# Optimization experiments

Hardware: AMD Instinct MI355X
Metric: run time of the kernel (lower is better)

Reference implementation:

```python
import jax, jax.numpy as jnp
import numpy as np

B, S, D, H = 32, 8192, 128, 256  # batch-of-MLPs, seq_len, emb_dim, hidden_dim
LN_EPS = 1e-5


def setup_inputs() -> dict:
    key = jax.random.key(0)
    k0, k1, k2, k3 = jax.random.split(key, 4)
    x = jax.random.normal(k0, (B, S, D), dtype=jnp.float32)
    # shared learned Q projection (torch Linear stores W as [out,in]; y = x @ W.T)
    Wq = jax.random.normal(k1, (D, D), dtype=jnp.float32) / np.float32(np.sqrt(D))
    # per-batch-index (non-shared) fast-weight MLP params
    W1 = jax.random.normal(k2, (B, D, H), dtype=jnp.float32) / np.float32(np.sqrt(D))
    b1 = jnp.zeros((B, H), dtype=jnp.float32)
    W2 = jax.random.normal(k3, (B, H, D), dtype=jnp.float32) / np.float32(np.sqrt(H))
    b2 = jnp.zeros((B, D), dtype=jnp.float32)
    gamma = jnp.ones((B, D), dtype=jnp.float32)
    beta = jnp.zeros((B, D), dtype=jnp.float32)
    return dict(x=x, Wq=Wq, W1=W1, b1=b1, W2=W2, b2=b2, gamma=gamma, beta=beta)


def reference(x, Wq, W1, b1, W2, b2, gamma, beta):
    # queries = silu(Q(x))
    q = jax.nn.silu(jnp.einsum('bsd,ed->bse', x, Wq))
    # torch F.normalize with default dim=1 -> L2-normalize over the sequence axis
    q = q / jnp.clip(jnp.linalg.norm(q, axis=1, keepdims=True), 1e-12)
    # ParallelMLPs: per-index MLP with distinct weights (grouped GEMM), + residual
    h = jax.nn.silu(jnp.einsum('bsd,bdh->bsh', q, W1) + b1[:, None, :])
    o = jnp.einsum('bsh,bhd->bsd', h, W2) + b2[:, None, :]
    mu = jnp.mean(o, axis=-1, keepdims=True)
    var = jnp.mean(jnp.square(o - mu), axis=-1, keepdims=True)
    ln = (o - mu) / jnp.sqrt(var + LN_EPS) * gamma[:, None, :] + beta[:, None, :]
    return ln + q
```

## Files before the change

### kernel.cpp

```cpp
#include <hip/hip_runtime.h>
#include <stdint.h>

#define B_ 32
#define S_ 8192
#define D_ 128
#define H_ 256

typedef __attribute__((ext_vector_type(4))) float f32x4;
typedef __attribute__((ext_vector_type(16))) float f32x16;
typedef __attribute__((ext_vector_type(8))) short bf16x8;
typedef __attribute__((ext_vector_type(4))) unsigned int u32x4;

__device__ __forceinline__ unsigned short f2bf(float f) {
    union { float f; unsigned int u; } v; v.f = f;
    unsigned int r = v.u + 0x7fffu + ((v.u >> 16) & 1u);
    return (unsigned short)(r >> 16);
}
__device__ __forceinline__ float bf2f(unsigned short u) {
    union { unsigned int u; float f; } v; v.u = ((unsigned int)u) << 16;
    return v.f;
}
__device__ __forceinline__ float silu_f(float v) {
    return v * __builtin_amdgcn_rcpf(1.0f + __expf(-v));
}
__device__ __forceinline__ unsigned int cvtpk(float lo, float hi) {
    unsigned int r;
    asm("v_cvt_pk_bf16_f32 %0, %1, %2" : "=v"(r) : "v"(lo), "v"(hi));
    return r;
}
__device__ __forceinline__ void plswap(unsigned int& a, unsigned int& b) {
    asm("v_permlane32_swap_b32 %0, %1" : "+v"(a), "+v"(b));
}
__device__ __forceinline__ void gl16(const void* g, void* l) {
    __builtin_amdgcn_global_load_lds(
        (const __attribute__((address_space(1))) unsigned int*)g,
        (__attribute__((address_space(3))) unsigned int*)l, 16, 0, 0);
}

__global__ void k_prep(const float* __restrict__ Wq, const float* __restrict__ W1,
                       const float* __restrict__ W2, const float* __restrict__ b1,
                       unsigned short* __restrict__ wq_img,
                       unsigned short* __restrict__ wpkg,
                       float* __restrict__ b1r) {
    __shared__ __align__(16) unsigned short tile[8192];
    int t = threadIdx.x, blk = blockIdx.x;
    if (blk < 128) {
        int b = blk >> 2, hc = blk & 3;
#pragma unroll
        for (int i = 0; i < 8; i++) {
            int idx = t + i * 256;
            int d = idx >> 4, hj = idx & 15;
            f32x4 v = *(const f32x4*)(W1 + ((size_t)(b * D_ + d)) * H_ + hc * 64 + hj * 4);
#pragma unroll
            for (int u = 0; u < 4; u++) tile[(hj * 4 + u) * 128 + d] = f2bf(v[u]);
        }
        __syncthreads();
        char* img = (char*)wpkg + (size_t)b * 131072 + (size_t)hc * 32768;
#pragma unroll
        for (int i = 0; i < 4; i++) {
            int c = t + i * 256;
            int n = c >> 9, kk = (c >> 6) & 7, l = c & 63;
            u32x4 v = *(const u32x4*)(tile + (n * 32 + (l & 31)) * 128 + kk * 16 + (l >> 5) * 8);
            *(u32x4*)(img + n * 16384 + kk * 1024 + l * 16) = v;
        }
    } else if (blk < 256) {
        int a = blk - 128;
        int b = a >> 2, hc = a & 3;
#pragma unroll
        for (int i = 0; i < 8; i++) {
            int idx = t + i * 256;
            int h = idx >> 5, d4 = idx & 31;
            f32x4 v = *(const f32x4*)(W2 + ((size_t)(b * H_ + hc * 64 + h)) * D_ + d4 * 4);
#pragma unroll
            for (int u = 0; u < 4; u++) tile[(d4 * 4 + u) * 64 + h] = f2bf(v[u]);
        }
        __syncthreads();
        char* img = (char*)wpkg + (size_t)b * 131072 + (size_t)hc * 32768;
#pragma unroll
        for (int i = 0; i < 4; i++) {
            int c = t + i * 256;
            int dn = c >> 8, n = (c >> 7) & 1, kk2 = (c >> 6) & 1, l = c & 63;
            u32x4 v = *(const u32x4*)(tile + (dn * 32 + (l & 31)) * 64 + n * 32 + kk2 * 16 + (l >> 5) * 8);
            *(u32x4*)(img + n * 16384 + 8192 + dn * 2048 + kk2 * 1024 + l * 16) = v;
        }
    } else if (blk < 260) {
        int base = (blk - 256) * 512;
#pragma unroll
        for (int i = 0; i < 2; i++) {
            int c = base + i * 256 + t;
            int n = c >> 9, kk = (c >> 6) & 7, l = c & 63;
            int e = n * 32 + (l & 31), d = kk * 16 + (l >> 5) * 8;
            f32x4 v0 = *(const f32x4*)(Wq + e * 128 + d);
            f32x4 v1 = *(const f32x4*)(Wq + e * 128 + d + 4);
            u32x4 o;
            o[0] = cvtpk(v0[0], v0[1]); o[1] = cvtpk(v0[2], v0[3]);
            o[2] = cvtpk(v1[0], v1[1]); o[3] = cvtpk(v1[2], v1[3]);
            *(u32x4*)((char*)wq_img + (size_t)c * 16) = o;
        }
    } else {
        int idx = (blk - 260) * 256 + t;
        int b = idx >> 8, rem = idx & 255;
        int hc = rem >> 6, n = (rem >> 5) & 1, hi = (rem >> 4) & 1, r = rem & 15;
        int h = hc * 64 + n * 32 + (r & 3) + 8 * (r >> 2) + 4 * hi;
        b1r[idx] = b1[b * H_ + h];
    }
}

__global__ __launch_bounds__(256, 1) void k_qproj(
        const float* __restrict__ x, const unsigned short* __restrict__ wq_img,
        unsigned short* __restrict__ q_img, float* __restrict__ part) {
    __shared__ __align__(16) char lds[34816];
    int tid = threadIdx.x;
    int lane = tid & 63, w = tid >> 6;
    int c31 = lane & 31, hi = lane >> 5;
    int blk = blockIdx.x;
    int b = blk >> 6, st = blk & 63;

#pragma unroll
    for (int i = 0; i < 8; i++) {
        int off = tid * 16 + i * 4096;
        gl16((const char*)wq_img + off, lds + off);
    }

    const float* xr = x + ((size_t)b * S_ + (size_t)st * 128 + w * 32 + c31) * D_;
    bf16x8 xf[8];
#pragma unroll
    for (int kk = 0; kk < 8; kk++) {
        f32x4 v0 = *(const f32x4*)(xr + kk * 16 + hi * 8);
        f32x4 v1 = *(const f32x4*)(xr + kk * 16 + hi * 8 + 4);
        union { unsigned int u[4]; bf16x8 v; } o;
        o.u[0] = cvtpk(v0[0], v0[1]); o.u[1] = cvtpk(v0[2], v0[3]);
        o.u[2] = cvtpk(v1[0], v1[1]); o.u[3] = cvtpk(v1[2], v1[3]);
        xf[kk] = o.v;
    }
    __syncthreads();

    size_t grp = (size_t)b * 256 + st * 4 + w;
    char* qo = (char*)q_img + grp * 8192;
    float* ssl = (float*)(lds + 32768 + w * 512);

#pragma unroll
    for (int n = 0; n < 4; n++) {
        f32x16 acch;
#pragma unroll
        for (int e = 0; e < 16; e++) acch[e] = 0.0f;
#pragma unroll
        for (int kk = 0; kk < 8; kk++) {
            bf16x8 wqf = *(const bf16x8*)(lds + n * 8192 + kk * 1024 + lane * 16);
            acch = __builtin_amdgcn_mfma_f32_32x32x16_bf16(wqf, xf[kk], acch, 0, 0, 0);
        }
        float sv[16];
#pragma unroll
        for (int r = 0; r < 16; r++) sv[r] = silu_f(acch[r]);
        unsigned int P[8];
#pragma unroll
        for (int pp = 0; pp < 8; pp++) P[pp] = cvtpk(sv[2 * pp], sv[2 * pp + 1]);
        plswap(P[0], P[2]); plswap(P[1], P[3]);
        plswap(P[4], P[6]); plswap(P[5], P[7]);
        union { unsigned int u[4]; bf16x8 v; } f0, f1;
        f0.u[0] = P[0]; f0.u[1] = P[1]; f0.u[2] = P[2]; f0.u[3] = P[3];
        f1.u[0] = P[4]; f1.u[1] = P[5]; f1.u[2] = P[6]; f1.u[3] = P[7];
        *(bf16x8*)(qo + (2 * n) * 1024 + lane * 16) = f0.v;
        *(bf16x8*)(qo + (2 * n + 1) * 1024 + lane * 16) = f1.v;
        float ssq[16];
#pragma unroll
        for (int r = 0; r < 16; r++) ssq[r] = sv[r] * sv[r];
#pragma unroll
        for (int r = 0; r < 16; r++) {
            ssq[r] += __shfl_xor(ssq[r], 1, 64);
            ssq[r] += __shfl_xor(ssq[r], 2, 64);
            ssq[r] += __shfl_xor(ssq[r], 4, 64);
            ssq[r] += __shfl_xor(ssq[r], 8, 64);
            ssq[r] += __shfl_xor(ssq[r], 16, 64);
        }
        if ((lane & 31) == 0) {
#pragma unroll
            for (int r = 0; r < 16; r++)
                ssl[n * 32 + (r & 3) + 8 * (r >> 2) + 4 * hi] = ssq[r];
        }
    }
    __syncthreads();
    if (tid < 128) {
        float s = *(const float*)(lds + 32768 + 0 * 512 + tid * 4) +
                  *(const float*)(lds + 32768 + 1 * 512 + tid * 4) +
                  *(const float*)(lds + 32768 + 2 * 512 + tid * 4) +
                  *(const float*)(lds + 32768 + 3 * 512 + tid * 4);
        part[((size_t)b * 64 + st) * 128 + tid] = s;
    }
}

__global__ void k_scalew(const float* __restrict__ part, unsigned short* __restrict__ wpkg,
                         float* __restrict__ scale) {
    __shared__ float sc_l[128];
    int blk = blockIdx.x;
    int b = blk >> 2;
    int t = threadIdx.x;
    if (t < 128) {
        const float* p = part + (size_t)b * 8192 + t;
        float s = 0.0f;
#pragma unroll 8
        for (int i = 0; i < 64; i++) s += p[i * 128];
        float sc = 1.0f / fmaxf(sqrtf(s), 1e-12f);
        sc_l[t] = sc;
        if ((blk & 3) == 0) scale[b * 128 + t] = sc;
    }
    __syncthreads();
    char* region = (char*)wpkg + (size_t)b * 131072 + (size_t)(blk & 3) * 32768;
#pragma unroll
    for (int i = 0; i < 4; i++) {
        int c = t + i * 256;
        int n = c >> 9, kk = (c >> 6) & 7, l = c & 63;
        char* addr = region + n * 16384 + kk * 1024 + l * 16;
        int d0 = kk * 16 + (l >> 5) * 8;
        u32x4 v = *(const u32x4*)addr;
        const unsigned short* pv = (const unsigned short*)&v;
        u32x4 o;
#pragma unroll
        for (int j = 0; j < 4; j++)
            o[j] = cvtpk(bf2f(pv[2 * j]) * sc_l[d0 + 2 * j],
                         bf2f(pv[2 * j + 1]) * sc_l[d0 + 2 * j + 1]);
        *(u32x4*)addr = o;
    }
}

__global__ __launch_bounds__(256, 2) void k_mlp(
        const unsigned short* __restrict__ q_img, const float* __restrict__ scale,
        const unsigned short* __restrict__ wpkg, const float* __restrict__ b1r,
        const float* __restrict__ b2, const float* __restrict__ gamma,
        const float* __restrict__ beta, float* __restrict__ out) {
    __shared__ __align__(16) char lds[33792];
    int tid = threadIdx.x;
    int lane = tid & 63, w = tid >> 6;
    int c31 = lane & 31, hi = lane >> 5;
    int blk = blockIdx.x;
    int k = blk & 7, j = blk >> 3;
    int b = k * 4 + (j >> 6);
    int st = j & 63;

    const char* wb = (const char*)wpkg + (size_t)b * 131072;
    size_t grp = (size_t)b * 256 + st * 4 + w;
    const char* qg = (const char*)q_img + grp * 8192;

    bf16x8 qf[8];
#pragma unroll
    for (int kk = 0; kk < 8; kk++)
        qf[kk] = *(const bf16x8*)(qg + kk * 1024 + lane * 16);

    gl16((const char*)b1r + (size_t)b * 1024 + lane * 16, lds + 32768);

#define STAGEPKG(p, slot) do {                                          \
    _Pragma("unroll")                                                   \
    for (int i_ = 0; i_ < 4; i_++) {                                    \
        int off_ = tid * 16 + i_ * 4096;                                \
        gl16(wb + (p) * 16384 + off_, lds + (slot) * 16384 + off_);     \
    } } while (0)

    STAGEPKG(0, 0);
    STAGEPKG(1, 1);

    f32x16 acco[4];
#pragma unroll
    for (int dn = 0; dn < 4; dn++)
#pragma unroll
        for (int e = 0; e < 16; e++) acco[dn][e] = 0.0f;

    const float* b1l = (const float*)(lds + 32768);

#pragma unroll
    for (int p = 0; p < 8; p++) {
        const int hc = p >> 1, n = p & 1, slot = p & 1;
        if (p == 7) { asm volatile("s_waitcnt vmcnt(0)" ::: "memory"); }
        else        { asm volatile("s_waitcnt vmcnt(4)" ::: "memory"); }
        __builtin_amdgcn_s_barrier();
        __builtin_amdgcn_sched_barrier(0);

        f32x16 acch;
        {
            const float* bp = b1l + (hc * 2 + n) * 32 + hi * 16;
#pragma unroll
            for (int jq = 0; jq < 4; jq++) {
                f32x4 bq = *(const f32x4*)(bp + jq * 4);
#pragma unroll
                for (int e = 0; e < 4; e++) acch[jq * 4 + e] = bq[e];
            }
        }
        const char* s0 = lds + slot * 16384;
#pragma unroll
        for (int kk = 0; kk < 8; kk++) {
            bf16x8 wf = *(const bf16x8*)(s0 + kk * 1024 + lane * 16);
            acch = __builtin_amdgcn_mfma_f32_32x32x16_bf16(wf, qf[kk], acch, 0, 0, 0);
        }
        float sv[16];
#pragma unroll
        for (int r = 0; r < 16; r++) sv[r] = silu_f(acch[r]);
        unsigned int P[8];
#pragma unroll
        for (int pp = 0; pp < 8; pp++) P[pp] = cvtpk(sv[2 * pp], sv[2 * pp + 1]);
        plswap(P[0], P[2]); plswap(P[1], P[3]);
        plswap(P[4], P[6]); plswap(P[5], P[7]);
        union { unsigned int u[4]; bf16x8 v; } f0, f1;
        f0.u[0] = P[0]; f0.u[1] = P[1]; f0.u[2] = P[2]; f0.u[3] = P[3];
        f1.u[0] = P[4]; f1.u[1] = P[5]; f1.u[2] = P[6]; f1.u[3] = P[7];
        bf16x8 pa0 = f0.v, pa1 = f1.v;
#pragma unroll
        for (int kk2 = 0; kk2 < 2; kk2++)
#pragma unroll
            for (int dn = 0; dn < 4; dn++) {
                bf16x8 wf2 = *(const bf16x8*)(s0 + 8192 + dn * 2048 + kk2 * 1024 + lane * 16);
                acco[dn] = __builtin_amdgcn_mfma_f32_32x32x16_bf16(kk2 ? pa1 : pa0, wf2,
                                                                   acco[dn], 0, 0, 0);
            }

        asm volatile("s_waitcnt lgkmcnt(0)" ::: "memory");
        __builtin_amdgcn_sched_barrier(0);
        __builtin_amdgcn_s_barrier();
        if (p < 6) STAGEPKG(p + 2, slot);
    }
#undef STAGEPKG

    __syncthreads();
    char* myq = (char*)lds + w * 8192;
#pragma unroll
    for (int kk = 0; kk < 8; kk++)
        *(bf16x8*)(myq + c31 * 256 + ((kk * 32 + hi * 16) ^ ((c31 & 7) << 4))) = qf[kk];

    float scv[4], gv[4], bev[4], b2v[4];
#pragma unroll
    for (int dn = 0; dn < 4; dn++) {
        int d = dn * 32 + c31;
        scv[dn] = scale[b * 128 + d];
        gv[dn]  = gamma[b * 128 + d];
        bev[dn] = beta[b * 128 + d];
        b2v[dn] = b2[b * 128 + d];
    }

    float* og = out + grp * 32 * 128;
#pragma unroll
    for (int r = 0; r < 16; r++) {
        float v0 = acco[0][r] + b2v[0], v1 = acco[1][r] + b2v[1];
        float v2 = acco[2][r] + b2v[2], v3 = acco[3][r] + b2v[3];
        float s1 = (v0 + v1) + (v2 + v3);
        float s2 = (v0 * v0 + v1 * v1) + (v2 * v2 + v3 * v3);
        s1 += __shfl_xor(s1, 1, 64);   s2 += __shfl_xor(s2, 1, 64);
        s1 += __shfl_xor(s1, 2, 64);   s2 += __shfl_xor(s2, 2, 64);
        s1 += __shfl_xor(s1, 4, 64);   s2 += __shfl_xor(s2, 4, 64);
        s1 += __shfl_xor(s1, 8, 64);   s2 += __shfl_xor(s2, 8, 64);
        s1 += __shfl_xor(s1, 16, 64);  s2 += __shfl_xor(s2, 16, 64);
        float mu = s1 * (1.0f / 128.0f);
        float var = s2 * (1.0f / 128.0f) - mu * mu;
        float rstd = rsqrtf(var + 1e-5f);
        int srow0 = (r & 3) + 8 * (r >> 2);
        int row = srow0 + 4 * hi;
        float vv[4] = {v0, v1, v2, v3};
#pragma unroll
        for (int dn = 0; dn < 4; dn++) {
            float qv = bf2f(*(const unsigned short*)(myq + row * 256 +
                        ((dn * 64 + c31 * 2) ^ ((row & 7) << 4)))) * scv[dn];
            float o = (vv[dn] - mu) * rstd * gv[dn] + bev[dn] + qv;
            og[(size_t)row * 128 + dn * 32 + c31] = o;
        }
    }
}

extern "C" void kernel_launch(void* const* d_in, const int* in_sizes, int n_in,
                              void* d_out, int out_size, void* d_ws, size_t ws_size,
                              hipStream_t stream) {
    (void)in_sizes; (void)n_in; (void)out_size; (void)ws_size;
    const float* x     = (const float*)d_in[0];
    const float* Wq    = (const float*)d_in[1];
    const float* W1    = (const float*)d_in[2];
    const float* b1    = (const float*)d_in[3];
    const float* W2    = (const float*)d_in[4];
    const float* b2    = (const float*)d_in[5];
    const float* gamma = (const float*)d_in[6];
    const float* beta  = (const float*)d_in[7];
    float* out = (float*)d_out;

    char* ws = (char*)d_ws;
    unsigned short* wq_img = (unsigned short*)(ws);
    unsigned short* wpkg   = (unsigned short*)(ws + 32768);
    float* part            = (float*)(ws + 4227072);
    float* scale           = (float*)(ws + 5275648);
    float* b1r             = (float*)(ws + 5292032);
    unsigned short* q_img  = (unsigned short*)(ws + 5324800);

    hipLaunchKernelGGL(k_prep, dim3(292), dim3(256), 0, stream, Wq, W1, W2, b1, wq_img, wpkg, b1r);
    hipLaunchKernelGGL(k_qproj, dim3(2048), dim3(256), 0, stream, x, wq_img, q_img, part);
    hipLaunchKernelGGL(k_scalew, dim3(128), dim3(256), 0, stream, part, wpkg, scale);
    hipLaunchKernelGGL(k_mlp, dim3(2048), dim3(256), 0, stream,
                       q_img, scale, wpkg, b1r, b2, gamma, beta, out);
}
```

Baseline: 127.1 us.

## Process two row groups per wave in k_mlp to reuse staged weights

Each wave in k_mlp now handles two 32-row groups instead of one. The grid is halved, and every LDS weight fragment feeds two MFMAs, so weight staging traffic and barrier overhead per row are halved. Launch bounds drop to one block per SM to make room for the doubled accumulators and q fragments. s_setprio is also raised around the MFMA sections. The cost is higher register pressure and lower occupancy, which may hurt latency hiding, and the epilogue now runs twice per wave.

```diff
diff --git a/kernel.cpp b/kernel.cpp
--- a/kernel.cpp
+++ b/kernel.cpp
@@ -223,7 +223,7 @@
     }
 }
 
-__global__ __launch_bounds__(256, 2) void k_mlp(
+__global__ __launch_bounds__(256, 1) void k_mlp(
         const unsigned short* __restrict__ q_img, const float* __restrict__ scale,
         const unsigned short* __restrict__ wpkg, const float* __restrict__ b1r,
         const float* __restrict__ b2, const float* __restrict__ gamma,
@@ -234,17 +234,20 @@
     int c31 = lane & 31, hi = lane >> 5;
     int blk = blockIdx.x;
     int k = blk & 7, j = blk >> 3;
-    int b = k * 4 + (j >> 6);
-    int st = j & 63;
+    int b = k * 4 + (j >> 5);
+    int st2 = j & 31;
 
     const char* wb = (const char*)wpkg + (size_t)b * 131072;
-    size_t grp = (size_t)b * 256 + st * 4 + w;
-    const char* qg = (const char*)q_img + grp * 8192;
-
-    bf16x8 qf[8];
-#pragma unroll
-    for (int kk = 0; kk < 8; kk++)
-        qf[kk] = *(const bf16x8*)(qg + kk * 1024 + lane * 16);
+    size_t g0 = (size_t)b * 256 + st2 * 8 + w * 2;
+    const char* qgA = (const char*)q_img + g0 * 8192;
+    const char* qgB = qgA + 8192;
+
+    bf16x8 qfA[8], qfB[8];
+#pragma unroll
+    for (int kk = 0; kk < 8; kk++) {
+        qfA[kk] = *(const bf16x8*)(qgA + kk * 1024 + lane * 16);
+        qfB[kk] = *(const bf16x8*)(qgB + kk * 1024 + lane * 16);
+    }
 
     gl16((const char*)b1r + (size_t)b * 1024 + lane * 16, lds + 32768);
 
@@ -258,11 +261,11 @@
     STAGEPKG(0, 0);
     STAGEPKG(1, 1);
 
-    f32x16 acco[4];
+    f32x16 accoA[4], accoB[4];
 #pragma unroll
     for (int dn = 0; dn < 4; dn++)
 #pragma unroll
-        for (int e = 0; e < 16; e++) acco[dn][e] = 0.0f;
+        for (int e = 0; e < 16; e++) { accoA[dn][e] = 0.0f; accoB[dn][e] = 0.0f; }
 
     const float* b1l = (const float*)(lds + 32768);
 
@@ -274,42 +277,70 @@
         __builtin_amdgcn_s_barrier();
         __builtin_amdgcn_sched_barrier(0);
 
-        f32x16 acch;
+        f32x16 acchA, acchB;
         {
             const float* bp = b1l + (hc * 2 + n) * 32 + hi * 16;
 #pragma unroll
             for (int jq = 0; jq < 4; jq++) {
                 f32x4 bq = *(const f32x4*)(bp + jq * 4);
 #pragma unroll
-                for (int e = 0; e < 4; e++) acch[jq * 4 + e] = bq[e];
+                for (int e = 0; e < 4; e++) {
+                    acchA[jq * 4 + e] = bq[e];
+                    acchB[jq * 4 + e] = bq[e];
+                }
             }
         }
         const char* s0 = lds + slot * 16384;
+        __builtin_amdgcn_s_setprio(1);
 #pragma unroll
         for (int kk = 0; kk < 8; kk++) {
             bf16x8 wf = *(const bf16x8*)(s0 + kk * 1024 + lane * 16);
-            acch = __builtin_amdgcn_mfma_f32_32x32x16_bf16(wf, qf[kk], acch, 0, 0, 0);
-        }
-        float sv[16];
-#pragma unroll
-        for (int r = 0; r < 16; r++) sv[r] = silu_f(acch[r]);
-        unsigned int P[8];
-#pragma unroll
-        for (int pp = 0; pp < 8; pp++) P[pp] = cvtpk(sv[2 * pp], sv[2 * pp + 1]);
-        plswap(P[0], P[2]); plswap(P[1], P[3]);
-        plswap(P[4], P[6]); plswap(P[5], P[7]);
-        union { unsigned int u[4]; bf16x8 v; } f0, f1;
-        f0.u[0] = P[0]; f0.u[1] = P[1]; f0.u[2] = P[2]; f0.u[3] = P[3];
-        f1.u[0] = P[4]; f1.u[1] = P[5]; f1.u[2] = P[6]; f1.u[3] = P[7];
-        bf16x8 pa0 = f0.v, pa1 = f1.v;
+            acchA = __builtin_amdgcn_mfma_f32_32x32x16_bf16(wf, qfA[kk], acchA, 0, 0, 0);
+            acchB = __builtin_amdgcn_mfma_f32_32x32x16_bf16(wf, qfB[kk], acchB, 0, 0, 0);
+        }
+        __builtin_amdgcn_s_setprio(0);
+        bf16x8 paA0, paA1, paB0, paB1;
+        {
+            float sv[16];
+#pragma unroll
+            for (int r = 0; r < 16; r++) sv[r] = silu_f(acchA[r]);
+            unsigned int P[8];
+#pragma unroll
+            for (int pp = 0; pp < 8; pp++) P[pp] = cvtpk(sv[2 * pp], sv[2 * pp + 1]);
+            plswap(P[0], P[2]); plswap(P[1], P[3]);
+            plswap(P[4], P[6]); plswap(P[5], P[7]);
+            union { unsigned int u[4]; bf16x8 v; } f0, f1;
+            f0.u[0] = P[0]; f0.u[1] = P[1]; f0.u[2] = P[2]; f0.u[3] = P[3];
+            f1.u[0] = P[4]; f1.u[1] = P[5]; f1.u[2] = P[6]; f1.u[3] = P[7];
+            paA0 = f0.v; paA1 = f1.v;
+        }
+        {
+            float sv[16];
+#pragma unroll
+            for (int r = 0; r < 16; r++) sv[r] = silu_f(acchB[r]);
+            unsigned int P[8];
+#pragma unroll
+            for (int pp = 0; pp < 8; pp++) P[pp] = cvtpk(sv[2 * pp], sv[2 * pp + 1]);
+            plswap(P[0], P[2]); plswap(P[1], P[3]);
+            plswap(P[4], P[6]); plswap(P[5], P[7]);
+            union { unsigned int u[4]; bf16x8 v; } f0, f1;
+            f0.u[0] = P[0]; f0.u[1] = P[1]; f0.u[2] = P[2]; f0.u[3] = P[3];
+            f1.u[0] = P[4]; f1.u[1] = P[5]; f1.u[2] = P[6]; f1.u[3] = P[7];
+            paB0 = f0.v; paB1 = f1.v;
+        }
+
+        __builtin_amdgcn_s_setprio(1);
 #pragma unroll
         for (int kk2 = 0; kk2 < 2; kk2++)
 #pragma unroll
             for (int dn = 0; dn < 4; dn++) {
                 bf16x8 wf2 = *(const bf16x8*)(s0 + 8192 + dn * 2048 + kk2 * 1024 + lane * 16);
-                acco[dn] = __builtin_amdgcn_mfma_f32_32x32x16_bf16(kk2 ? pa1 : pa0, wf2,
-                                                                   acco[dn], 0, 0, 0);
+                accoA[dn] = __builtin_amdgcn_mfma_f32_32x32x16_bf16(kk2 ? paA1 : paA0, wf2,
+                                                                    accoA[dn], 0, 0, 0);
+                accoB[dn] = __builtin_amdgcn_mfma_f32_32x32x16_bf16(kk2 ? paB1 : paB0, wf2,
+                                                                    accoB[dn], 0, 0, 0);
             }
+        __builtin_amdgcn_s_setprio(0);
 
         asm volatile("s_waitcnt lgkmcnt(0)" ::: "memory");
         __builtin_amdgcn_sched_barrier(0);
@@ -320,9 +351,6 @@
 
     __syncthreads();
     char* myq = (char*)lds + w * 8192;
-#pragma unroll
-    for (int kk = 0; kk < 8; kk++)
-        *(bf16x8*)(myq + c31 * 256 + ((kk * 32 + hi * 16) ^ ((c31 & 7) << 4))) = qf[kk];
 
     float scv[4], gv[4], bev[4], b2v[4];
 #pragma unroll
@@ -334,32 +362,40 @@
         b2v[dn] = b2[b * 128 + d];
     }
 
-    float* og = out + grp * 32 * 128;
-#pragma unroll
-    for (int r = 0; r < 16; r++) {
-        float v0 = acco[0][r] + b2v[0], v1 = acco[1][r] + b2v[1];
-        float v2 = acco[2][r] + b2v[2], v3 = acco[3][r] + b2v[3];
-        float s1 = (v0 + v1) + (v2 + v3);
-        float s2 = (v0 * v0 + v1 * v1) + (v2 * v2 + v3 * v3);
-        s1 += __shfl_xor(s1, 1, 64);   s2 += __shfl_xor(s2, 1, 64);
-        s1 += __shfl_xor(s1, 2, 64);   s2 += __shfl_xor(s2, 2, 64);
-        s1 += __shfl_xor(s1, 4, 64);   s2 += __shfl_xor(s2, 4, 64);
-        s1 += __shfl_xor(s1, 8, 64);   s2 += __shfl_xor(s2, 8, 64);
-        s1 += __shfl_xor(s1, 16, 64);  s2 += __shfl_xor(s2, 16, 64);
-        float mu = s1 * (1.0f / 128.0f);
-        float var = s2 * (1.0f / 128.0f) - mu * mu;
-        float rstd = rsqrtf(var + 1e-5f);
-        int srow0 = (r & 3) + 8 * (r >> 2);
-        int row = srow0 + 4 * hi;
-        float vv[4] = {v0, v1, v2, v3};
-#pragma unroll
-        for (int dn = 0; dn < 4; dn++) {
-            float qv = bf2f(*(const unsigned short*)(myq + row * 256 +
-                        ((dn * 64 + c31 * 2) ^ ((row & 7) << 4)))) * scv[dn];
-            float o = (vv[dn] - mu) * rstd * gv[dn] + bev[dn] + qv;
-            og[(size_t)row * 128 + dn * 32 + c31] = o;
-        }
-    }
+#define EPILOG(QF, ACCO, GRP) do {                                              \
+    _Pragma("unroll")                                                           \
+    for (int kk = 0; kk < 8; kk++)                                              \
+        *(bf16x8*)(myq + c31 * 256 + ((kk * 32 + hi * 16) ^ ((c31 & 7) << 4))) = QF[kk]; \
+    float* og = out + (GRP) * 32 * 128;                                         \
+    _Pragma("unroll")                                                           \
+    for (int r = 0; r < 16; r++) {                                              \
+        float v0 = ACCO[0][r] + b2v[0], v1 = ACCO[1][r] + b2v[1];               \
+        float v2 = ACCO[2][r] + b2v[2], v3 = ACCO[3][r] + b2v[3];               \
+        float s1 = (v0 + v1) + (v2 + v3);                                       \
+        float s2 = (v0 * v0 + v1 * v1) + (v2 * v2 + v3 * v3);                   \
+        s1 += __shfl_xor(s1, 1, 64);   s2 += __shfl_xor(s2, 1, 64);             \
+        s1 += __shfl_xor(s1, 2, 64);   s2 += __shfl_xor(s2, 2, 64);             \
+        s1 += __shfl_xor(s1, 4, 64);   s2 += __shfl_xor(s2, 4, 64);             \
+        s1 += __shfl_xor(s1, 8, 64);   s2 += __shfl_xor(s2, 8, 64);             \
+        s1 += __shfl_xor(s1, 16, 64);  s2 += __shfl_xor(s2, 16, 64);            \
+        float mu = s1 * (1.0f / 128.0f);                                        \
+        float var = s2 * (1.0f / 128.0f) - mu * mu;                             \
+        float rstd = rsqrtf(var + 1e-5f);                                       \
+        int srow0 = (r & 3) + 8 * (r >> 2);                                     \
+        int row = srow0 + 4 * hi;                                               \
+        float vv[4] = {v0, v1, v2, v3};                                         \
+        _Pragma("unroll")                                                       \
+        for (int dn = 0; dn < 4; dn++) {                                        \
+            float qv = bf2f(*(const unsigned short*)(myq + row * 256 +          \
+                        ((dn * 64 + c31 * 2) ^ ((row & 7) << 4)))) * scv[dn];   \
+            float o = (vv[dn] - mu) * rstd * gv[dn] + bev[dn] + qv;             \
+            og[(size_t)row * 128 + dn * 32 + c31] = o;                          \
+        }                                                                       \
+    } } while (0)
+
+    EPILOG(qfA, accoA, g0);
+    EPILOG(qfB, accoB, (g0 + 1));
+#undef EPILOG
 }
 
 extern "C" void kernel_launch(void* const* d_in, const int* in_sizes, int n_in,
@@ -387,6 +423,6 @@
     hipLaunchKernelGGL(k_prep, dim3(292), dim3(256), 0, stream, Wq, W1, W2, b1, wq_img, wpkg, b1r);
     hipLaunchKernelGGL(k_qproj, dim3(2048), dim3(256), 0, stream, x, wq_img, q_img, part);
     hipLaunchKernelGGL(k_scalew, dim3(128), dim3(256), 0, stream, part, wpkg, scale);
-    hipLaunchKernelGGL(k_mlp, dim3(2048), dim3(256), 0, stream,
+    hipLaunchKernelGGL(k_mlp, dim3(1024), dim3(256), 0, stream,
                        q_img, scale, wpkg, b1r, b2, gamma, beta, out);
 }
```

Result: slower. 156.6 us (+23.2%).
